# Kernel optimization log

Hardware: AMD Instinct MI355X
Metric: run time of the kernel (lower is better)

## Reference

```python
import jax, jax.numpy as jnp
import numpy as np
import math

EPS = 1e-5

def layernorm(x, w):
    mu = jnp.mean(x, axis=-1, keepdims=True)
    var = jnp.var(x, axis=-1, keepdims=True)
    return (x - mu) * jax.lax.rsqrt(var + EPS) * w

def setup_inputs() -> dict:
    key = jax.random.key(0)
    ks = jax.random.split(key, 6)
    B, T, C = 2, 2048, 768
    s = 0.02
    return {
        "x": jax.random.normal(ks[0], (B, T, C), jnp.float32),
        "w_ln1": jnp.ones((C,), jnp.float32),
        "w_attn": jax.random.normal(ks[1], (C, 3 * C), jnp.float32) * s,
        "w_attn_proj": jax.random.normal(ks[2], (C, C), jnp.float32) * s,
        "w_ln2": jnp.ones((C,), jnp.float32),
        "w_fc": jax.random.normal(ks[3], (C, 4 * C), jnp.float32) * s,
        "w_mlp_proj": jax.random.normal(ks[4], (4 * C, C), jnp.float32) * s,
    }

def _attention(x, w_attn, w_attn_proj, n_head):
    B, T, C = x.shape
    D = C // n_head
    qkv = x @ w_attn  # [B,T,3C]
    q, k, v = jnp.split(qkv, 3, axis=-1)
    # [B,H,T,D]
    q = q.reshape(B, T, n_head, D).transpose(0, 2, 1, 3)
    k = k.reshape(B, T, n_head, D).transpose(0, 2, 1, 3)
    v = v.reshape(B, T, n_head, D).transpose(0, 2, 1, 3)
    # squared L2 distance via ||q||^2 + ||k||^2 - 2 q.k (same math, no [B,H,T,T,D] tensor)
    q2 = jnp.sum(q * q, axis=-1)  # [B,H,T]
    k2 = jnp.sum(k * k, axis=-1)  # [B,H,T]
    qk = jnp.einsum('bhqd,bhkd->bhqk', q, k)
    sq_l2 = q2[..., :, None] + k2[..., None, :] - 2.0 * qk  # [B,H,T,T]
    scale = -1.0 / (2.0 * math.sqrt(D))
    scores = jnp.exp(sq_l2 * scale)
    causal = jnp.tril(jnp.ones((T, T), bool))
    scores = jnp.where(causal[None, None], scores, 0.0)
    y = jnp.einsum('bhqk,bhkd->bhqd', scores, v)
    y = y.transpose(0, 2, 1, 3).reshape(B, T, C)
    return y @ w_attn_proj

def reference(x, w_ln1, w_attn, w_attn_proj, w_ln2, w_fc, w_mlp_proj):
    n_head = 12
    x = x + _attention(layernorm(x, w_ln1), w_attn, w_attn_proj, n_head)
    h = layernorm(x, w_ln2)
    h = jax.nn.gelu(h @ w_fc, approximate=False) @ w_mlp_proj
    return x + h
```

## Files before the change

### kernel.cpp

```cpp
#include <hip/hip_runtime.h>

typedef unsigned short u16;
typedef unsigned int u32;
typedef short bf16x8 __attribute__((ext_vector_type(8)));
typedef float f32x4 __attribute__((ext_vector_type(4)));

#define AS1 __attribute__((address_space(1)))
#define AS3 __attribute__((address_space(3)))

__device__ __forceinline__ float bf2f(u16 u){ return __uint_as_float(((u32)u)<<16); }
__device__ __forceinline__ u16 f2bf(float f){
  u32 x = __float_as_uint(f);
  x += 0x7fffu + ((x>>16)&1u);
  return (u16)(x>>16);
}
__device__ __forceinline__ float gelu_exact(float x){
  return 0.5f*x*(1.f + erff(x*0.7071067811865475f));
}

__global__ __launch_bounds__(256) void transpose_cast(
    const float* __restrict__ w, u16* __restrict__ wt, int K, int N)
{
  __shared__ float t[32][33];
  int lx = threadIdx.x & 31, ly = threadIdx.x >> 5;
  int n0 = blockIdx.x*32, k0 = blockIdx.y*32;
  #pragma unroll
  for (int j=0;j<4;j++) t[ly+j*8][lx] = w[(long)(k0+ly+j*8)*N + n0+lx];
  __syncthreads();
  #pragma unroll
  for (int j=0;j<4;j++) wt[(long)(n0+ly+j*8)*K + k0+lx] = f2bf(t[lx][ly+j*8]);
}

__global__ __launch_bounds__(256) void ln_rows(
    const float* __restrict__ x, const float* __restrict__ w, u16* __restrict__ out)
{
  int row = blockIdx.x, tid = threadIdx.x;
  const float* xr = x + (long)row*768;
  float v0 = xr[tid], v1 = xr[tid+256], v2 = xr[tid+512];
  float s = v0+v1+v2, sq = v0*v0+v1*v1+v2*v2;
  #pragma unroll
  for (int o=32;o>=1;o>>=1){ s += __shfl_down(s,o); sq += __shfl_down(sq,o); }
  __shared__ float red[8];
  int wv = tid>>6, ln = tid&63;
  if (ln==0){ red[wv]=s; red[wv+4]=sq; }
  __syncthreads();
  float S  = red[0]+red[1]+red[2]+red[3];
  float SQ = red[4]+red[5]+red[6]+red[7];
  float mu = S*(1.f/768.f);
  float var = SQ*(1.f/768.f) - mu*mu;
  float rstd = rsqrtf(var + 1e-5f);
  u16* o = out + (long)row*768;
  o[tid]     = f2bf((v0-mu)*rstd*w[tid]);
  o[tid+256] = f2bf((v1-mu)*rstd*w[tid+256]);
  o[tid+512] = f2bf((v2-mu)*rstd*w[tid+512]);
}

__global__ __launch_bounds__(256) void v_transpose(
    const u16* __restrict__ qkv, u16* __restrict__ vt)
{
  __shared__ __align__(16) u16 t[64*72];
  int b = blockIdx.z, h = blockIdx.y, t0 = blockIdx.x*64;
  int tid = threadIdx.x;
  int r = tid>>2, g = tid&3, c8 = g*16;
  const u16* src = qkv + ((long)(b*2048 + t0 + r))*2304 + 1536 + h*64 + c8;
  int wcol = c8 ^ (((r>>4)&3)*16);
  *(uint4*)&t[r*72 + wcol]     = *(const uint4*)src;
  *(uint4*)&t[r*72 + wcol + 8] = *(const uint4*)(src + 8);
  __syncthreads();
  int d = r;
  int rcol = d ^ (g*16);
  u32 pk[8];
  #pragma unroll
  for (int j=0;j<8;j++){
    u32 lo = t[(c8+2*j  )*72 + rcol];
    u32 hi = t[(c8+2*j+1)*72 + rcol];
    pk[j] = lo | (hi<<16);
  }
  u16* dst = vt + ((long)((b*12+h)*64 + d))*2048 + t0 + c8;
  uint4 o0 = {pk[0],pk[1],pk[2],pk[3]};
  uint4 o1 = {pk[4],pk[5],pk[6],pk[7]};
  *(uint4*)dst       = o0;
  *(uint4*)(dst + 8) = o1;
}

template<int EPI>
__global__ __launch_bounds__(256) void gemm_bt(
    const u16* __restrict__ A, const u16* __restrict__ BT,
    int M, int N, int K,
    u16* __restrict__ outB,
    float* __restrict__ q2g, float* __restrict__ k2g)
{
  __shared__ __align__(16) u16 As[128*32];
  __shared__ __align__(16) u16 Bs[128*32];
  int tid = threadIdx.x;
  int gx = gridDim.x;
  int nwg = gx * gridDim.y;
  int flat = blockIdx.x + gx*blockIdx.y;
  int cpx = nwg >> 3;
  int swz = (flat & 7)*cpx + (flat >> 3);
  int n0 = (swz % gx)*128, m0 = (swz / gx)*128;
  int w = tid>>6, lane = tid&63, lr = lane&15, lg = lane>>4;
  int wr = w>>1, wc = w&1;
  f32x4 acc[4][4];
  f32x4 z = {0.f,0.f,0.f,0.f};
  #pragma unroll
  for (int m=0;m<4;m++)
    #pragma unroll
    for (int n=0;n<4;n++) acc[m][n] = z;
  int rr16 = lane>>2, cc = (lane&3)*8;
  const u16* gA0 = A  + (long)(m0 + (2*w  )*16 + rr16)*K + cc;
  const u16* gA1 = A  + (long)(m0 + (2*w+1)*16 + rr16)*K + cc;
  const u16* gB0 = BT + (long)(n0 + (2*w  )*16 + rr16)*K + cc;
  const u16* gB1 = BT + (long)(n0 + (2*w+1)*16 + rr16)*K + cc;
  u16* lA0 = As + (2*w  )*512;
  u16* lA1 = As + (2*w+1)*512;
  u16* lB0 = Bs + (2*w  )*512;
  u16* lB1 = Bs + (2*w+1)*512;
  for (int k0=0; k0<K; k0+=32){
    __builtin_amdgcn_global_load_lds((const AS1 void*)gA0, (AS3 void*)lA0, 16, 0, 0);
    __builtin_amdgcn_global_load_lds((const AS1 void*)gA1, (AS3 void*)lA1, 16, 0, 0);
    __builtin_amdgcn_global_load_lds((const AS1 void*)gB0, (AS3 void*)lB0, 16, 0, 0);
    __builtin_amdgcn_global_load_lds((const AS1 void*)gB1, (AS3 void*)lB1, 16, 0, 0);
    gA0 += 32; gA1 += 32; gB0 += 32; gB1 += 32;
    __syncthreads();
    bf16x8 af[4], bfr[4];
    #pragma unroll
    for (int m=0;m<4;m++) af[m]  = *(const bf16x8*)&As[(wr*64+m*16+lr)*32 + lg*8];
    #pragma unroll
    for (int n=0;n<4;n++) bfr[n] = *(const bf16x8*)&Bs[(wc*64+n*16+lr)*32 + lg*8];
    #pragma unroll
    for (int m=0;m<4;m++)
      #pragma unroll
      for (int n=0;n<4;n++)
        acc[m][n] = __builtin_amdgcn_mfma_f32_16x16x32_bf16(af[m], bfr[n], acc[m][n], 0,0,0);
    __syncthreads();
  }
  if (EPI==0){
    #pragma unroll
    for (int m=0;m<4;m++){
      float s2[4] = {0.f,0.f,0.f,0.f};
      #pragma unroll
      for (int n=0;n<4;n++)
        #pragma unroll
        for (int r=0;r<4;r++){
          int row = m0 + wr*64 + m*16 + lg*4 + r;
          int col = n0 + wc*64 + n*16 + lr;
          u16 ub = f2bf(acc[m][n][r]);
          outB[(long)row*N + col] = ub;
          float vr = bf2f(ub);
          s2[r] += vr*vr;
        }
      #pragma unroll
      for (int r=0;r<4;r++){
        float t = s2[r];
        t += __shfl_xor(t,1); t += __shfl_xor(t,2); t += __shfl_xor(t,4); t += __shfl_xor(t,8);
        if (lr==0){
          int head = (n0 + wc*64) >> 6;
          int row = m0 + wr*64 + m*16 + lg*4 + r;
          int bb = row >> 11, tt = row & 2047;
          if (head < 12)      q2g[((long)(bb*12 + head     ))*2048 + tt] = t;
          else if (head < 24) k2g[((long)(bb*12 + head - 12))*2048 + tt] = t;
        }
      }
    }
  } else {
    #pragma unroll
    for (int m=0;m<4;m++)
      #pragma unroll
      for (int n=0;n<4;n++)
        #pragma unroll
        for (int r=0;r<4;r++){
          int row = m0 + wr*64 + m*16 + lg*4 + r;
          int col = n0 + wc*64 + n*16 + lr;
          outB[(long)row*N + col] = f2bf(gelu_exact(acc[m][n][r]));
        }
  }
}

__global__ __launch_bounds__(256) void gemm_ks(
    const u16* __restrict__ A, const u16* __restrict__ BT,
    int M, int N, int K, int KS,
    float* __restrict__ pb)
{
  __shared__ __align__(16) u16 As[128*32];
  __shared__ __align__(16) u16 Bs[64*32];
  int tid = threadIdx.x;
  int n0 = blockIdx.x*64, m0 = blockIdx.y*128;
  int kbeg = blockIdx.z*KS;
  int w = tid>>6, lane = tid&63, lr = lane&15, lg = lane>>4;
  int wr = w>>1, wc = w&1;
  f32x4 acc[4][2];
  f32x4 z = {0.f,0.f,0.f,0.f};
  #pragma unroll
  for (int m=0;m<4;m++){ acc[m][0]=z; acc[m][1]=z; }
  int rr16 = lane>>2, cc = (lane&3)*8;
  const u16* gA0 = A  + (long)(m0 + (2*w  )*16 + rr16)*K + kbeg + cc;
  const u16* gA1 = A  + (long)(m0 + (2*w+1)*16 + rr16)*K + kbeg + cc;
  const u16* gB0 = BT + (long)(n0 + w*16 + rr16)*K + kbeg + cc;
  u16* lA0 = As + (2*w  )*512;
  u16* lA1 = As + (2*w+1)*512;
  u16* lB0 = Bs + w*512;
  for (int k0=0; k0<KS; k0+=32){
    __builtin_amdgcn_global_load_lds((const AS1 void*)gA0, (AS3 void*)lA0, 16, 0, 0);
    __builtin_amdgcn_global_load_lds((const AS1 void*)gA1, (AS3 void*)lA1, 16, 0, 0);
    __builtin_amdgcn_global_load_lds((const AS1 void*)gB0, (AS3 void*)lB0, 16, 0, 0);
    gA0 += 32; gA1 += 32; gB0 += 32;
    __syncthreads();
    bf16x8 af[4], bfr[2];
    #pragma unroll
    for (int m=0;m<4;m++) af[m]  = *(const bf16x8*)&As[(wr*64+m*16+lr)*32 + lg*8];
    #pragma unroll
    for (int n=0;n<2;n++) bfr[n] = *(const bf16x8*)&Bs[(wc*32+n*16+lr)*32 + lg*8];
    #pragma unroll
    for (int m=0;m<4;m++)
      #pragma unroll
      for (int n=0;n<2;n++)
        acc[m][n] = __builtin_amdgcn_mfma_f32_16x16x32_bf16(af[m], bfr[n], acc[m][n], 0,0,0);
    __syncthreads();
  }
  long zofs = (long)blockIdx.z*M*N;
  #pragma unroll
  for (int m=0;m<4;m++)
    #pragma unroll
    for (int n=0;n<2;n++)
      #pragma unroll
      for (int r=0;r<4;r++){
        int row = m0 + wr*64 + m*16 + lg*4 + r;
        int col = n0 + wc*32 + n*16 + lr;
        pb[zofs + (long)row*N + col] = acc[m][n][r];
      }
}

__global__ __launch_bounds__(256) void reduce2(
    const float* __restrict__ p, const float* __restrict__ resid,
    float* __restrict__ out, long n)
{
  long i = ((long)blockIdx.x*256 + threadIdx.x)*4;
  f32x4 a = *(const f32x4*)(resid+i);
  f32x4 b = *(const f32x4*)(p+i);
  f32x4 c = *(const f32x4*)(p+n+i);
  *(f32x4*)(out+i) = a+b+c;
}

__global__ __launch_bounds__(128) void attn_fused(
    const u16* __restrict__ qkv, const u16* __restrict__ vt,
    const float* __restrict__ q2g, const float* __restrict__ k2g,
    u16* __restrict__ Y)
{
  constexpr int C3=2304, C=768, T=2048, PADP=72;
  __shared__ __align__(16) u16 Ks[2][4096];
  __shared__ __align__(16) u16 Vs[2][4096];
  __shared__ __align__(16) u16 Ps[2][16*PADP];
  int bz = blockIdx.x;
  int swzb = (bz&7)*96 + (bz>>3);
  int sp = swzb & 31;
  int hh = (swzb>>5) % 12;
  int b  = swzb / 384;
  int tid = threadIdx.x, w = tid>>6, lane = tid&63, lr = lane&15, lg = lane>>4;
  long base = (long)b*T;
  long bh = (long)(b*12 + hh);
  const u16* kbase = qkv + base*C3 + C + hh*64;
  const u16* vbase = vt + bh*64*(long)T;
  const float* k2p = k2g + bh*T;
  const float* q2p0 = q2g + bh*T;

  int rowl = lane>>3;
  int c16 = (lane&7) ^ rowl;
  const u16* kp[4]; const u16* vp[4];
  #pragma unroll
  for (int i=0;i<4;i++){
    int c = w*4 + i;
    kp[i] = kbase + (long)(c*8 + rowl)*C3 + c16*8;
    vp[i] = vbase + (long)(c*8 + rowl)*T + c16*8;
  }
  u16* Pw = &Ps[w][0];
  f32x4 z = {0.f,0.f,0.f,0.f};

  for (int ph=0; ph<2; ++ph){
    int s = ph ? 63 - sp : sp;
    int ktl = s>>1;
    int qg0 = s*32 + w*16;
    const u16* qrow = qkv + (base + qg0 + lr)*C3 + hh*64;
    bf16x8 aq0 = *(const bf16x8*)(qrow + lg*8);
    bf16x8 aq1 = *(const bf16x8*)(qrow + 32 + lg*8);
    float q2m[4]; int qg[4];
    #pragma unroll
    for (int rr=0;rr<4;rr++){
      qg[rr] = qg0 + lg*4 + rr;
      q2m[rr] = 0.0625f * q2p0[qg[rr]];
    }
    f32x4 accY[4];
    #pragma unroll
    for (int i=0;i<4;i++) accY[i] = z;

    #pragma unroll
    for (int i=0;i<4;i++){
      __builtin_amdgcn_global_load_lds((const AS1 void*)kp[i], (AS3 void*)&Ks[0][(w*4+i)*512], 16, 0, 0);
      __builtin_amdgcn_global_load_lds((const AS1 void*)vp[i], (AS3 void*)&Vs[0][(w*4+i)*512], 16, 0, 0);
    }
    float k2n[4];
    #pragma unroll
    for (int nf=0;nf<4;nf++) k2n[nf] = k2p[nf*16+lr];
    __syncthreads();

    int cur = 0;
    for (int kt=0; kt<=ktl; ++kt){
      float k2c[4];
      #pragma unroll
      for (int i=0;i<4;i++) k2c[i] = k2n[i];
      if (kt < ktl){
        long kadd = (long)(kt+1)*64*C3;
        long vadd = (long)(kt+1)*64;
        #pragma unroll
        for (int i=0;i<4;i++){
          __builtin_amdgcn_global_load_lds((const AS1 void*)(kp[i]+kadd), (AS3 void*)&Ks[cur^1][(w*4+i)*512], 16, 0, 0);
          __builtin_amdgcn_global_load_lds((const AS1 void*)(vp[i]+vadd), (AS3 void*)&Vs[cur^1][(w*4+i)*512], 16, 0, 0);
        }
        #pragma unroll
        for (int nf=0;nf<4;nf++) k2n[nf] = k2p[(kt+1)*64 + nf*16+lr];
      }
      const u16* Kc = &Ks[cur][0];
      const u16* Vc = &Vs[cur][0];
      int kg0 = kt*64;
      #pragma unroll
      for (int nf=0;nf<4;nf++){
        int row = nf*16 + lr;
        int sw0 = ((lg    ) ^ (row&7))*8;
        int sw1 = ((4 | lg) ^ (row&7))*8;
        f32x4 sc = z;
        sc = __builtin_amdgcn_mfma_f32_16x16x32_bf16(aq0, *(const bf16x8*)&Kc[row*64 + sw0], sc, 0,0,0);
        sc = __builtin_amdgcn_mfma_f32_16x16x32_bf16(aq1, *(const bf16x8*)&Kc[row*64 + sw1], sc, 0,0,0);
        int kg = kg0 + row;
        float k2m = 0.0625f * k2c[nf];
        #pragma unroll
        for (int rr=0;rr<4;rr++){
          float e = __expf(0.125f*sc[rr] - q2m[rr] - k2m);
          e = (kg <= qg[rr]) ? e : 0.f;
          Pw[(lg*4+rr)*PADP + row] = f2bf(e);
        }
      }
      __builtin_amdgcn_wave_barrier();
      asm volatile("s_waitcnt lgkmcnt(0)" ::: "memory");
      bf16x8 ap0 = *(const bf16x8*)&Pw[lr*PADP + lg*8];
      bf16x8 ap1 = *(const bf16x8*)&Pw[lr*PADP + 32 + lg*8];
      #pragma unroll
      for (int nf=0;nf<4;nf++){
        int row = nf*16 + lr;
        int sw0 = ((lg    ) ^ (row&7))*8;
        int sw1 = ((4 | lg) ^ (row&7))*8;
        accY[nf] = __builtin_amdgcn_mfma_f32_16x16x32_bf16(ap0, *(const bf16x8*)&Vc[row*64 + sw0], accY[nf], 0,0,0);
        accY[nf] = __builtin_amdgcn_mfma_f32_16x16x32_bf16(ap1, *(const bf16x8*)&Vc[row*64 + sw1], accY[nf], 0,0,0);
      }
      __syncthreads();
      cur ^= 1;
    }
    #pragma unroll
    for (int nf=0;nf<4;nf++)
      #pragma unroll
      for (int rr=0;rr<4;rr++)
        Y[(base + qg0 + lg*4 + rr)*C + hh*64 + nf*16 + lr] = f2bf(accY[nf][rr]);
  }
}

extern "C" void kernel_launch(void* const* d_in, const int* in_sizes, int n_in,
                              void* d_out, int out_size, void* d_ws, size_t ws_size,
                              hipStream_t stream)
{
  (void)in_sizes; (void)n_in; (void)out_size; (void)ws_size;
  const float* x      = (const float*)d_in[0];
  const float* w_ln1  = (const float*)d_in[1];
  const float* w_attn = (const float*)d_in[2];
  const float* w_ap   = (const float*)d_in[3];
  const float* w_ln2  = (const float*)d_in[4];
  const float* w_fc   = (const float*)d_in[5];
  const float* w_mlp  = (const float*)d_in[6];
  float* out = (float*)d_out;
  const int M = 4096, T = 2048;
  const long NROW = (long)M*768;

  u16* ws      = (u16*)d_ws;
  u16* wT_attn = ws;
  u16* wT_ap   = wT_attn + 2304*768;
  u16* wT_fc   = wT_ap   + 768*768;
  u16* wT_mlp  = wT_fc   + 3072*768;
  u16* xln     = wT_mlp  + 768*3072;
  u16* qkvb    = xln     + 4096*768;
  u16* Ybuf    = qkvb    + 4096*2304;
  u16* hbuf    = qkvb;
  float* x2    = (float*)(Ybuf + 4096*768);
  u16* vtb     = (u16*)(x2 + 4096*768);
  float* q2g   = (float*)(vtb + 2*12*64*2048);
  float* k2g   = q2g + 24*2048;
  float* pbuf  = k2g + 24*2048;

  dim3 blk(256);
  transpose_cast<<<dim3(2304/32,  768/32), blk, 0, stream>>>(w_attn, wT_attn,  768, 2304);
  transpose_cast<<<dim3( 768/32,  768/32), blk, 0, stream>>>(w_ap,   wT_ap,    768,  768);
  transpose_cast<<<dim3(3072/32,  768/32), blk, 0, stream>>>(w_fc,   wT_fc,    768, 3072);
  transpose_cast<<<dim3( 768/32, 3072/32), blk, 0, stream>>>(w_mlp,  wT_mlp,  3072,  768);

  ln_rows<<<dim3(M), blk, 0, stream>>>(x, w_ln1, xln);
  gemm_bt<0><<<dim3(2304/128, M/128), blk, 0, stream>>>(xln, wT_attn, M, 2304, 768, qkvb, q2g, k2g);
  v_transpose<<<dim3(T/64, 12, 2), blk, 0, stream>>>(qkvb, vtb);
  attn_fused<<<dim3(2*12*32), dim3(128), 0, stream>>>(qkvb, vtb, q2g, k2g, Ybuf);
  gemm_ks<<<dim3(768/64, M/128, 2), blk, 0, stream>>>(Ybuf, wT_ap, M, 768, 768, 384, pbuf);
  reduce2<<<dim3(NROW/1024), blk, 0, stream>>>(pbuf, x, x2, NROW);
  ln_rows<<<dim3(M), blk, 0, stream>>>(x2, w_ln2, xln);
  gemm_bt<1><<<dim3(3072/128, M/128), blk, 0, stream>>>(xln, wT_fc, M, 3072, 768, hbuf, nullptr, nullptr);
  gemm_ks<<<dim3(768/64, M/128, 2), blk, 0, stream>>>(hbuf, wT_mlp, M, 768, 3072, 1536, pbuf);
  reduce2<<<dim3(NROW/1024), blk, 0, stream>>>(pbuf, x2, out, NROW);
}
```

Measured before the change: 304.7 us.

## Double-buffer LDS tiles in bf16 GEMM kernels to overlap loads with MFMA

Both GEMM kernels (gemm_bt and the split-K gemm_ks) now use two LDS buffers per operand. Each iteration issues the global-to-LDS loads for the next K tile before computing on the current one, and the first tile is prefetched before the loop. This drops the barrier that sat between issuing the loads and computing, so memory latency can hide behind MFMA work. The cost is double the LDS per workgroup, which may lower occupancy. If the compiler waits on outstanding LDS-DMA loads before the ds_reads, the intended overlap may not happen.

New measurement: 297.0 us. 2.5% less time.

```diff
diff --git a/kernel.cpp b/kernel.cpp
--- a/kernel.cpp
+++ b/kernel.cpp
@@ -90,8 +90,8 @@
     u16* __restrict__ outB,
     float* __restrict__ q2g, float* __restrict__ k2g)
 {
-  __shared__ __align__(16) u16 As[128*32];
-  __shared__ __align__(16) u16 Bs[128*32];
+  __shared__ __align__(16) u16 As[2][128*32];
+  __shared__ __align__(16) u16 Bs[2][128*32];
   int tid = threadIdx.x;
   int gx = gridDim.x;
   int nwg = gx * gridDim.y;
@@ -112,28 +112,37 @@
   const u16* gA1 = A  + (long)(m0 + (2*w+1)*16 + rr16)*K + cc;
   const u16* gB0 = BT + (long)(n0 + (2*w  )*16 + rr16)*K + cc;
   const u16* gB1 = BT + (long)(n0 + (2*w+1)*16 + rr16)*K + cc;
-  u16* lA0 = As + (2*w  )*512;
-  u16* lA1 = As + (2*w+1)*512;
-  u16* lB0 = Bs + (2*w  )*512;
-  u16* lB1 = Bs + (2*w+1)*512;
+  int o0 = (2*w)*512, o1 = (2*w+1)*512;
+  __builtin_amdgcn_global_load_lds((const AS1 void*)gA0, (AS3 void*)(&As[0][o0]), 16, 0, 0);
+  __builtin_amdgcn_global_load_lds((const AS1 void*)gA1, (AS3 void*)(&As[0][o1]), 16, 0, 0);
+  __builtin_amdgcn_global_load_lds((const AS1 void*)gB0, (AS3 void*)(&Bs[0][o0]), 16, 0, 0);
+  __builtin_amdgcn_global_load_lds((const AS1 void*)gB1, (AS3 void*)(&Bs[0][o1]), 16, 0, 0);
+  gA0 += 32; gA1 += 32; gB0 += 32; gB1 += 32;
+  __syncthreads();
+  int cur = 0;
   for (int k0=0; k0<K; k0+=32){
-    __builtin_amdgcn_global_load_lds((const AS1 void*)gA0, (AS3 void*)lA0, 16, 0, 0);
-    __builtin_amdgcn_global_load_lds((const AS1 void*)gA1, (AS3 void*)lA1, 16, 0, 0);
-    __builtin_amdgcn_global_load_lds((const AS1 void*)gB0, (AS3 void*)lB0, 16, 0, 0);
-    __builtin_amdgcn_global_load_lds((const AS1 void*)gB1, (AS3 void*)lB1, 16, 0, 0);
-    gA0 += 32; gA1 += 32; gB0 += 32; gB1 += 32;
-    __syncthreads();
+    if (k0+32 < K){
+      int nx = cur^1;
+      __builtin_amdgcn_global_load_lds((const AS1 void*)gA0, (AS3 void*)(&As[nx][o0]), 16, 0, 0);
+      __builtin_amdgcn_global_load_lds((const AS1 void*)gA1, (AS3 void*)(&As[nx][o1]), 16, 0, 0);
+      __builtin_amdgcn_global_load_lds((const AS1 void*)gB0, (AS3 void*)(&Bs[nx][o0]), 16, 0, 0);
+      __builtin_amdgcn_global_load_lds((const AS1 void*)gB1, (AS3 void*)(&Bs[nx][o1]), 16, 0, 0);
+      gA0 += 32; gA1 += 32; gB0 += 32; gB1 += 32;
+    }
+    const u16* Ac = As[cur];
+    const u16* Bc = Bs[cur];
     bf16x8 af[4], bfr[4];
     #pragma unroll
-    for (int m=0;m<4;m++) af[m]  = *(const bf16x8*)&As[(wr*64+m*16+lr)*32 + lg*8];
-    #pragma unroll
-    for (int n=0;n<4;n++) bfr[n] = *(const bf16x8*)&Bs[(wc*64+n*16+lr)*32 + lg*8];
+    for (int m=0;m<4;m++) af[m]  = *(const bf16x8*)&Ac[(wr*64+m*16+lr)*32 + lg*8];
+    #pragma unroll
+    for (int n=0;n<4;n++) bfr[n] = *(const bf16x8*)&Bc[(wc*64+n*16+lr)*32 + lg*8];
     #pragma unroll
     for (int m=0;m<4;m++)
       #pragma unroll
       for (int n=0;n<4;n++)
         acc[m][n] = __builtin_amdgcn_mfma_f32_16x16x32_bf16(af[m], bfr[n], acc[m][n], 0,0,0);
     __syncthreads();
+    cur ^= 1;
   }
   if (EPI==0){
     #pragma unroll
@@ -182,8 +191,8 @@
     int M, int N, int K, int KS,
     float* __restrict__ pb)
 {
-  __shared__ __align__(16) u16 As[128*32];
-  __shared__ __align__(16) u16 Bs[64*32];
+  __shared__ __align__(16) u16 As[2][128*32];
+  __shared__ __align__(16) u16 Bs[2][64*32];
   int tid = threadIdx.x;
   int n0 = blockIdx.x*64, m0 = blockIdx.y*128;
   int kbeg = blockIdx.z*KS;
@@ -197,26 +206,35 @@
   const u16* gA0 = A  + (long)(m0 + (2*w  )*16 + rr16)*K + kbeg + cc;
   const u16* gA1 = A  + (long)(m0 + (2*w+1)*16 + rr16)*K + kbeg + cc;
   const u16* gB0 = BT + (long)(n0 + w*16 + rr16)*K + kbeg + cc;
-  u16* lA0 = As + (2*w  )*512;
-  u16* lA1 = As + (2*w+1)*512;
-  u16* lB0 = Bs + w*512;
+  int oa0 = (2*w)*512, oa1 = (2*w+1)*512, ob = w*512;
+  __builtin_amdgcn_global_load_lds((const AS1 void*)gA0, (AS3 void*)(&As[0][oa0]), 16, 0, 0);
+  __builtin_amdgcn_global_load_lds((const AS1 void*)gA1, (AS3 void*)(&As[0][oa1]), 16, 0, 0);
+  __builtin_amdgcn_global_load_lds((const AS1 void*)gB0, (AS3 void*)(&Bs[0][ob ]), 16, 0, 0);
+  gA0 += 32; gA1 += 32; gB0 += 32;
+  __syncthreads();
+  int cur = 0;
   for (int k0=0; k0<KS; k0+=32){
-    __builtin_amdgcn_global_load_lds((const AS1 void*)gA0, (AS3 void*)lA0, 16, 0, 0);
-    __builtin_amdgcn_global_load_lds((const AS1 void*)gA1, (AS3 void*)lA1, 16, 0, 0);
-    __builtin_amdgcn_global_load_lds((const AS1 void*)gB0, (AS3 void*)lB0, 16, 0, 0);
-    gA0 += 32; gA1 += 32; gB0 += 32;
-    __syncthreads();
+    if (k0+32 < KS){
+      int nx = cur^1;
+      __builtin_amdgcn_global_load_lds((const AS1 void*)gA0, (AS3 void*)(&As[nx][oa0]), 16, 0, 0);
+      __builtin_amdgcn_global_load_lds((const AS1 void*)gA1, (AS3 void*)(&As[nx][oa1]), 16, 0, 0);
+      __builtin_amdgcn_global_load_lds((const AS1 void*)gB0, (AS3 void*)(&Bs[nx][ob ]), 16, 0, 0);
+      gA0 += 32; gA1 += 32; gB0 += 32;
+    }
+    const u16* Ac = As[cur];
+    const u16* Bc = Bs[cur];
     bf16x8 af[4], bfr[2];
     #pragma unroll
-    for (int m=0;m<4;m++) af[m]  = *(const bf16x8*)&As[(wr*64+m*16+lr)*32 + lg*8];
-    #pragma unroll
-    for (int n=0;n<2;n++) bfr[n] = *(const bf16x8*)&Bs[(wc*32+n*16+lr)*32 + lg*8];
+    for (int m=0;m<4;m++) af[m]  = *(const bf16x8*)&Ac[(wr*64+m*16+lr)*32 + lg*8];
+    #pragma unroll
+    for (int n=0;n<2;n++) bfr[n] = *(const bf16x8*)&Bc[(wc*32+n*16+lr)*32 + lg*8];
     #pragma unroll
     for (int m=0;m<4;m++)
       #pragma unroll
       for (int n=0;n<2;n++)
         acc[m][n] = __builtin_amdgcn_mfma_f32_16x16x32_bf16(af[m], bfr[n], acc[m][n], 0,0,0);
     __syncthreads();
+    cur ^= 1;
   }
   long zofs = (long)blockIdx.z*M*N;
   #pragma unroll
```
